# Kernel optimization log

Measured on AMD Instinct MI355X. Metric: run time of the kernel, lower is better.

## Reference

```python
import jax, jax.numpy as jnp
import numpy as np

COMMIT_LAMBDA = 0.25


def setup_inputs() -> dict:
    key = jax.random.key(0)
    k1, k2 = jax.random.split(key)
    B, C, T = 8, 256, 1024
    NCB, K, D = 2, 8192, 128
    x = jax.random.normal(k1, (B, C, T), dtype=jnp.float32)
    # EMA codebook weights buffer (init: randn * 0.1)
    codebooks = jax.random.normal(k2, (NCB, K, D), dtype=jnp.float32) * 0.1
    return {"x": x, "codebooks": codebooks}


def reference(x, codebooks):
    B, C, T = x.shape
    ncb, K, d = codebooks.shape
    # [B, C, T] -> [B*T, ncb, d]
    xs = x.reshape(B, ncb, d, T).transpose(0, 3, 1, 2).reshape(B * T, ncb, d)
    # squared euclidean distances (argmin-equivalent to cdist)
    x2 = jnp.sum(xs * xs, axis=-1)[..., None]            # [N, ncb, 1]
    c2 = jnp.sum(codebooks * codebooks, axis=-1)[None]    # [1, ncb, K]
    xc = jnp.einsum('bnd,nkd->bnk', xs, codebooks)        # [N, ncb, K]
    d2 = x2 - 2.0 * xc + c2
    idx = jnp.argmin(d2, axis=-1)                         # [N, ncb] int
    # gather nearest code vectors: [N, ncb, d]
    q = codebooks[jnp.arange(ncb)[None, :], idx]
    # straight-through estimator
    q_st = xs + jax.lax.stop_gradient(q - xs)
    # commitment loss (training mode): sum over codebooks of mse(x_i, q_i.detach())
    loss = COMMIT_LAMBDA * jnp.sum(
        jnp.mean((xs - jax.lax.stop_gradient(q)) ** 2, axis=(0, 2))
    )
    # reassemble to [B, C, T]
    quantized = q_st.reshape(B, T, ncb, d).transpose(0, 2, 3, 1).reshape(B, C, T)
    indices = idx.reshape(B, T, ncb).transpose(0, 2, 1)   # [B, ncb, T]
    return quantized, indices, loss
```

## Files before the change

### kernel.cpp

```cpp
#include <hip/hip_runtime.h>
#include <hip/hip_bf16.h>

#define BB   8
#define TT   1024
#define NCBN 2
#define DD   128
#define KK   8192
#define MM   8192

constexpr int OUT_IDX_OFF  = BB * 256 * TT;
constexpr int OUT_LOSS_OFF = OUT_IDX_OFF + BB * NCBN * TT;

#define THR   0.45f
#define QCAP  2048

typedef __attribute__((ext_vector_type(8))) short   short8;
typedef __attribute__((ext_vector_type(4))) float   float4v;

__device__ __forceinline__ unsigned short f2bf(float v) {
    unsigned u = __float_as_uint(v);
    return (unsigned short)((u + 0x7FFFu + ((u >> 16) & 1u)) >> 16);
}

__device__ __forceinline__ unsigned short f2bf_dn(float v) {
    unsigned u = __float_as_uint(v);
    unsigned short h = (unsigned short)(u >> 16);
    if ((u & 0x80000000u) && (u & 0xFFFFu)) ++h;
    return h;
}

__device__ __forceinline__ void gl_lds16(const void* g, void* l) {
    __builtin_amdgcn_global_load_lds(
        (const __attribute__((address_space(1))) unsigned int*)g,
        (__attribute__((address_space(3))) unsigned int*)l, 16, 0, 0);
}

__global__ __launch_bounds__(256)
void pack_x_kernel(const float* __restrict__ x, unsigned short* __restrict__ xbf,
                   float* __restrict__ x2, unsigned long long* __restrict__ pmin) {
    __shared__ float Ld[DD][65];
    const int b = blockIdx.x >> 1, n = blockIdx.x & 1;
    const int t0 = blockIdx.y * 64;
    const int tid = threadIdx.x;

    const float* base = x + ((size_t)(b * 256 + n * 128)) * TT + t0;
    const int dro = tid >> 2, q4 = tid & 3;
#pragma unroll
    for (int half = 0; half < 2; ++half) {
        int d = dro + half * 64;
        const float* rp = base + (size_t)d * TT + q4 * 16;
#pragma unroll
        for (int j = 0; j < 4; ++j) {
            float4 v = *(const float4*)(rp + j * 4);
            int t = q4 * 16 + j * 4;
            Ld[d][t + 0] = v.x; Ld[d][t + 1] = v.y;
            Ld[d][t + 2] = v.z; Ld[d][t + 3] = v.w;
        }
    }
    __syncthreads();

    if (tid < 64) {
        float s = 0.f;
        for (int d = 0; d < DD; ++d) { float v = Ld[d][tid]; s = fmaf(v, v, s); }
        x2[(size_t)n * MM + b * TT + t0 + tid] = s;
        pmin[(size_t)n * MM + b * TT + t0 + tid] = 0xFFFFFFFFFFFFFFFFull;
    }

    unsigned short* orow0 = xbf + ((size_t)n * MM + b * TT + t0) * DD;
#pragma unroll
    for (int pp = 0; pp < 4; ++pp) {
        int u = tid + pp * 256;
        int tt = u >> 4, sg = u & 15;
        unsigned short tmp[8];
#pragma unroll
        for (int j = 0; j < 8; ++j) tmp[j] = f2bf(Ld[sg * 8 + j][tt]);
        uint4 pk;
        pk.x = (unsigned)tmp[0] | ((unsigned)tmp[1] << 16);
        pk.y = (unsigned)tmp[2] | ((unsigned)tmp[3] << 16);
        pk.z = (unsigned)tmp[4] | ((unsigned)tmp[5] << 16);
        pk.w = (unsigned)tmp[6] | ((unsigned)tmp[7] << 16);
        *(uint4*)(orow0 + (size_t)tt * DD + sg * 8) = pk;
    }
}

__global__ __launch_bounds__(256)
void pack_c_kernel(const float* __restrict__ cb, unsigned short* __restrict__ cbf,
                   float* __restrict__ c2, float* __restrict__ out) {
    int g = blockIdx.x * 256 + threadIdx.x;
    if (g == 0) out[OUT_LOSS_OFF] = 0.f;
    const float4* crow = (const float4*)(cb + (size_t)g * DD);
    unsigned short* orow = cbf + (size_t)g * DD;
    float s = 0.f;
#pragma unroll 4
    for (int i2 = 0; i2 < 16; ++i2) {
        float4 v0 = crow[2 * i2];
        float4 v1 = crow[2 * i2 + 1];
        s = fmaf(v0.x, v0.x, s); s = fmaf(v0.y, v0.y, s);
        s = fmaf(v0.z, v0.z, s); s = fmaf(v0.w, v0.w, s);
        s = fmaf(v1.x, v1.x, s); s = fmaf(v1.y, v1.y, s);
        s = fmaf(v1.z, v1.z, s); s = fmaf(v1.w, v1.w, s);
        uint4 pk;
        pk.x = (unsigned)f2bf(v0.x) | ((unsigned)f2bf(v0.y) << 16);
        pk.y = (unsigned)f2bf(v0.z) | ((unsigned)f2bf(v0.w) << 16);
        pk.z = (unsigned)f2bf(v1.x) | ((unsigned)f2bf(v1.y) << 16);
        pk.w = (unsigned)f2bf(v1.z) | ((unsigned)f2bf(v1.w) << 16);
        *(uint4*)(orow + i2 * 8) = pk;
    }
    c2[g] = s;
}

__device__ void rescore_one(int n, int m, int k,
                            const float* __restrict__ x, const float* __restrict__ cb,
                            const float* __restrict__ x2, const float* __restrict__ c2,
                            unsigned long long* __restrict__ pmin) {
    int b = m >> 10, t = m & (TT - 1);
    const float* xp = x + ((size_t)(b * 256 + n * 128)) * TT + t;
    const float* cp = cb + ((size_t)(n * KK + k)) * DD;
    float xc = 0.f;
    for (int d = 0; d < DD; ++d)
        xc = fmaf(xp[(size_t)d * TT], cp[d], xc);
    float u = x2[n * MM + m] - 2.0f * xc;
    float s = u + c2[n * KK + k];
    unsigned long long pk = ((unsigned long long)__float_as_uint(s) << 32) | (unsigned)k;
    atomicMin(pmin + (size_t)n * MM + m, pk);
}

__global__ __launch_bounds__(512, 4)
void screen_kernel(const unsigned short* __restrict__ xbf,
                   const unsigned short* __restrict__ cbf,
                   const float* __restrict__ c2,
                   const float* __restrict__ x,
                   const float* __restrict__ cb32,
                   const float* __restrict__ x2,
                   unsigned long long* __restrict__ pmin) {
    __shared__ __align__(16) unsigned short Csh[2][128 * 128];
    __shared__ float          c2s[2][128];
    __shared__ unsigned int   minU[128];
    __shared__ unsigned int   qcnt;
    __shared__ unsigned int   queue[QCAP];
    __shared__ unsigned short queueY[QCAP];

    const int tid = threadIdx.x;
    const int id  = blockIdx.x;
    const int n   = id & 1;
    const int ks  = (id >> 1) & 3;
    const int qt  = id >> 3;
    const int m0  = qt * 128;
    const int k0  = ks * 2048;

    const int wave = tid >> 6, lane = tid & 63;
    const int cw = wave & 1, qw = wave >> 1;
    const int quad = lane >> 4, l15 = lane & 15;

    int goff[4];
#pragma unroll
    for (int p = 0; p < 4; ++p) {
        int u   = (p * 8 + wave) * 64 + lane;
        int row = u >> 4;
        int seg = (u & 15) ^ (row & 15);
        goff[p] = (row * DD + seg * 8) * 2;
    }

    const char*  asrc0 = (const char*)(cbf + ((size_t)n * KK + k0) * DD);
    const float* c2p   = c2 + (size_t)n * KK + k0;

    {
        const char* qsrc = (const char*)(xbf + ((size_t)n * MM + m0) * DD);
#pragma unroll
        for (int p = 0; p < 4; ++p)
            gl_lds16(qsrc + goff[p], &Csh[0][(p * 8 + wave) * 512]);
#pragma unroll
        for (int p = 0; p < 4; ++p)
            gl_lds16(asrc0 + goff[p], &Csh[1][(p * 8 + wave) * 512]);
    }
    if (tid < 32)  *(float4*)&c2s[1][tid * 4] = *(const float4*)(c2p + tid * 4);
    if (tid < 128) minU[tid] = 0xFFFFFFFFu;
    if (tid == 0)  qcnt = 0;
    __syncthreads();

    short8 bfr[2][4];
#pragma unroll
    for (int tq = 0; tq < 2; ++tq) {
        int q = qw * 32 + tq * 16 + l15;
#pragma unroll
        for (int k4 = 0; k4 < 4; ++k4) {
            int seg = k4 * 4 + quad;
            bfr[tq][k4] = *(const short8*)(&Csh[0][q * 128 + ((seg ^ l15) * 8)]);
        }
    }
    __syncthreads();

    float thr[2] = {3.4e38f, 3.4e38f};

    for (int it = 0; it <= 16; ++it) {
        const int sb   = it & 1;
        const int cbuf = sb ^ 1;
        const int dcur = (it < 16) ? it : 0;

        if (it < 16) {
            const int dn = (it + 1 < 16) ? (it + 1) : 0;
            const char* src = asrc0 + (size_t)dn * (128 * DD * 2);
#pragma unroll
            for (int p = 0; p < 4; ++p)
                gl_lds16(src + goff[p], &Csh[sb][(p * 8 + wave) * 512]);
            if (tid < 32)
                *(float4*)&c2s[sb][tid * 4] =
                    *(const float4*)(c2p + dn * 128 + tid * 4);
        }

        float4v acc[4][2];
#pragma unroll
        for (int tc = 0; tc < 4; ++tc)
#pragma unroll
            for (int tq = 0; tq < 2; ++tq)
                acc[tc][tq] = (float4v){0.f, 0.f, 0.f, 0.f};

#pragma unroll
        for (int k4 = 0; k4 < 4; ++k4) {
            short8 a[4];
#pragma unroll
            for (int tc = 0; tc < 4; ++tc) {
                int r = cw * 64 + tc * 16 + l15;
                int seg = k4 * 4 + quad;
                a[tc] = *(const short8*)(&Csh[cbuf][r * 128 + ((seg ^ l15) * 8)]);
            }
#pragma unroll
            for (int tc = 0; tc < 4; ++tc)
#pragma unroll
                for (int tq = 0; tq < 2; ++tq)
                    acc[tc][tq] = __builtin_amdgcn_mfma_f32_16x16x32_bf16(
                        a[tc], bfr[tq][k4], acc[tc][tq], 0, 0, 0);
        }

        float cmin[2] = {3.4e38f, 3.4e38f};
        const bool enq = (it > 0);
#pragma unroll
        for (int tc = 0; tc < 4; ++tc) {
            float4v c2r = *(const float4v*)(&c2s[cbuf][cw * 64 + tc * 16 + quad * 4]);
#pragma unroll
            for (int tq = 0; tq < 2; ++tq) {
                float y0 = fmaf(-2.0f, acc[tc][tq][0], c2r[0]);
                float y1 = fmaf(-2.0f, acc[tc][tq][1], c2r[1]);
                float y2 = fmaf(-2.0f, acc[tc][tq][2], c2r[2]);
                float y3 = fmaf(-2.0f, acc[tc][tq][3], c2r[3]);
                float m4 = fminf(fminf(y0, y1), fminf(y2, y3));
                cmin[tq] = fminf(cmin[tq], m4);
                if (enq && m4 <= thr[tq]) {
                    float yv[4] = {y0, y1, y2, y3};
#pragma unroll
                    for (int rg = 0; rg < 4; ++rg) {
                        if (yv[rg] <= thr[tq]) {
                            unsigned idx  = atomicAdd(&qcnt, 1u);
                            unsigned code = (unsigned)(dcur * 128 + cw * 64 + tc * 16 + quad * 4 + rg);
                            unsigned q    = (unsigned)(qw * 32 + tq * 16 + l15);
                            if (idx < QCAP) {
                                queue[idx]  = (q << 11) | code;
                                queueY[idx] = f2bf_dn(yv[rg]);
                            } else {
                                rescore_one(n, m0 + (int)q, k0 + (int)code,
                                            x, cb32, x2, c2, pmin);
                            }
                        }
                    }
                }
            }
        }

        if (it < 16) {
#pragma unroll
            for (int tq = 0; tq < 2; ++tq) {
                float v = cmin[tq];
                v = fminf(v, __shfl_xor(v, 16, 64));
                v = fminf(v, __shfl_xor(v, 32, 64));
                if (quad == 0) {
                    unsigned u  = __float_as_uint(v);
                    unsigned mu = (u & 0x80000000u) ? ~u : (u | 0x80000000u);
                    atomicMin(&minU[qw * 32 + tq * 16 + l15], mu);
                }
            }
        }
        __syncthreads();
        if (it < 16) {
#pragma unroll
            for (int tq = 0; tq < 2; ++tq) {
                unsigned mu = minU[qw * 32 + tq * 16 + l15];
                unsigned u  = (mu & 0x80000000u) ? (mu & 0x7FFFFFFFu) : ~mu;
                thr[tq] = __uint_as_float(u) + THR;
            }
        }
    }

    unsigned total = qcnt; if (total > QCAP) total = QCAP;
    for (unsigned i = tid; i < total; i += 512) {
        unsigned ent = queue[i];
        unsigned q   = ent >> 11;
        unsigned mu  = minU[q];
        unsigned u   = (mu & 0x80000000u) ? (mu & 0x7FFFFFFFu) : ~mu;
        float thrF   = __uint_as_float(u) + THR;
        float yv     = __uint_as_float((unsigned)queueY[i] << 16);
        if (yv <= thrF)
            rescore_one(n, m0 + (int)q, k0 + (int)(ent & 2047u),
                        x, cb32, x2, c2, pmin);
    }
}

__global__ __launch_bounds__(256)
void gather_kernel(const float* __restrict__ x, const float* __restrict__ cb,
                   const unsigned long long* __restrict__ pmin,
                   float* __restrict__ out) {
    __shared__ float Cr[64][DD + 1];
    __shared__ int   kid[64];
    const int b = blockIdx.x >> 1, n = blockIdx.x & 1;
    const int t0 = blockIdx.y * 64;
    const int tid = threadIdx.x;

    if (tid < 64) {
        int t = t0 + tid;
        int k = (int)(pmin[(size_t)n * MM + b * TT + t] & 0xFFFFFFFFull);
        kid[tid] = k;
        out[OUT_IDX_OFF + (b * NCBN + n) * TT + t] = (float)k;
    }
    __syncthreads();

    {
        int row = tid >> 2, q4 = tid & 3;
        const float* cp = cb + ((size_t)n * KK + kid[row]) * DD + q4 * 32;
#pragma unroll
        for (int j = 0; j < 8; ++j) {
            float4 v = *(const float4*)(cp + j * 4);
            int d = q4 * 32 + j * 4;
            Cr[row][d + 0] = v.x; Cr[row][d + 1] = v.y;
            Cr[row][d + 2] = v.z; Cr[row][d + 3] = v.w;
        }
    }
    __syncthreads();

    float lsum = 0.f;
    const float* xb = x  + ((size_t)(b * 256 + n * 128)) * TT + t0;
    float*       ob = out + ((size_t)(b * 256 + n * 128)) * TT + t0;
#pragma unroll
    for (int pp = 0; pp < 8; ++pp) {
        int u  = tid + pp * 256;
        int d  = u >> 4, ts = (u & 15) * 4;
        float4 xv = *(const float4*)(xb + (size_t)d * TT + ts);
        float4 qv = { Cr[ts + 0][d], Cr[ts + 1][d], Cr[ts + 2][d], Cr[ts + 3][d] };
        *(float4*)(ob + (size_t)d * TT + ts) = qv;
        float e;
        e = xv.x - qv.x; lsum = fmaf(e, e, lsum);
        e = xv.y - qv.y; lsum = fmaf(e, e, lsum);
        e = xv.z - qv.z; lsum = fmaf(e, e, lsum);
        e = xv.w - qv.w; lsum = fmaf(e, e, lsum);
    }

#pragma unroll
    for (int o = 32; o > 0; o >>= 1) lsum += __shfl_down(lsum, o, 64);
    __shared__ float wsum[4];
    int lane = tid & 63, w = tid >> 6;
    if (lane == 0) wsum[w] = lsum;
    __syncthreads();
    if (tid == 0) {
        float tot = wsum[0] + wsum[1] + wsum[2] + wsum[3];
        atomicAdd(out + OUT_LOSS_OFF, tot * 2.384185791015625e-7f);
    }
}

extern "C" void kernel_launch(void* const* d_in, const int* in_sizes, int n_in,
                              void* d_out, int out_size, void* d_ws, size_t ws_size,
                              hipStream_t stream) {
    (void)in_sizes; (void)n_in; (void)out_size; (void)ws_size;
    const float* x  = (const float*)d_in[0];
    const float* cb = (const float*)d_in[1];
    float* out = (float*)d_out;

    char* ws = (char*)d_ws;
    unsigned short* xbf = (unsigned short*)(ws);
    unsigned short* cbf = (unsigned short*)(ws + (4u << 20));
    float* x2 = (float*)(ws + (8u << 20));
    float* c2 = (float*)(ws + (8u << 20) + (64u << 10));
    unsigned long long* pmin =
        (unsigned long long*)(ws + (8u << 20) + (128u << 10));

    pack_x_kernel<<<dim3(16, 16), 256, 0, stream>>>(x, xbf, x2, pmin);
    pack_c_kernel<<<dim3(64), 256, 0, stream>>>(cb, cbf, c2, out);

    screen_kernel<<<dim3(512), 512, 0, stream>>>(xbf, cbf, c2, x, cb, x2, pmin);
    gather_kernel<<<dim3(16, 16), 256, 0, stream>>>(x, cb, pmin, out);
}
```

Baseline: 191.0 us.

## Fuse pack kernels, tighten per-tile threshold, drop pipeline tail, spill queue overflow

Merges the x and codebook packing kernels into one launch. In the screen kernel, each tile's scores are computed first and reduced to a per-tile minimum, so candidates are filtered against min(running threshold, tile min + margin) from the first tile onward instead of skipping enqueue on the first pass. The extra 17th loop iteration is removed. Queue overflow now goes to a per-block global spill buffer instead of immediate fp32 rescoring. The aim is fewer candidates to rescore and one less launch, at the cost of holding scores in registers and adding spill-buffer global traffic.

```diff
diff --git a/kernel.cpp b/kernel.cpp
--- a/kernel.cpp
+++ b/kernel.cpp
@@ -13,6 +13,7 @@
 
 #define THR   0.45f
 #define QCAP  2048
+#define SCAP  2048
 
 typedef __attribute__((ext_vector_type(8))) short   short8;
 typedef __attribute__((ext_vector_type(4))) float   float4v;
@@ -36,77 +37,80 @@
 }
 
 __global__ __launch_bounds__(256)
-void pack_x_kernel(const float* __restrict__ x, unsigned short* __restrict__ xbf,
-                   float* __restrict__ x2, unsigned long long* __restrict__ pmin) {
+void pack_kernel(const float* __restrict__ x, const float* __restrict__ cb,
+                 unsigned short* __restrict__ xbf, unsigned short* __restrict__ cbf,
+                 float* __restrict__ x2, float* __restrict__ c2,
+                 unsigned long long* __restrict__ pmin, float* __restrict__ out) {
     __shared__ float Ld[DD][65];
-    const int b = blockIdx.x >> 1, n = blockIdx.x & 1;
-    const int t0 = blockIdx.y * 64;
+    const int gb  = blockIdx.x;
     const int tid = threadIdx.x;
 
-    const float* base = x + ((size_t)(b * 256 + n * 128)) * TT + t0;
-    const int dro = tid >> 2, q4 = tid & 3;
-#pragma unroll
-    for (int half = 0; half < 2; ++half) {
-        int d = dro + half * 64;
-        const float* rp = base + (size_t)d * TT + q4 * 16;
-#pragma unroll
-        for (int j = 0; j < 4; ++j) {
-            float4 v = *(const float4*)(rp + j * 4);
-            int t = q4 * 16 + j * 4;
-            Ld[d][t + 0] = v.x; Ld[d][t + 1] = v.y;
-            Ld[d][t + 2] = v.z; Ld[d][t + 3] = v.w;
-        }
-    }
-    __syncthreads();
-
-    if (tid < 64) {
+    if (gb < 256) {
+        const int bxn = gb & 15, ty = gb >> 4;
+        const int b = bxn >> 1, n = bxn & 1;
+        const int t0 = ty * 64;
+
+        const float* base = x + ((size_t)(b * 256 + n * 128)) * TT + t0;
+        const int dro = tid >> 2, q4 = tid & 3;
+#pragma unroll
+        for (int half = 0; half < 2; ++half) {
+            int d = dro + half * 64;
+            const float* rp = base + (size_t)d * TT + q4 * 16;
+#pragma unroll
+            for (int j = 0; j < 4; ++j) {
+                float4 v = *(const float4*)(rp + j * 4);
+                int t = q4 * 16 + j * 4;
+                Ld[d][t + 0] = v.x; Ld[d][t + 1] = v.y;
+                Ld[d][t + 2] = v.z; Ld[d][t + 3] = v.w;
+            }
+        }
+        __syncthreads();
+
+        if (tid < 64) {
+            float s = 0.f;
+            for (int d = 0; d < DD; ++d) { float v = Ld[d][tid]; s = fmaf(v, v, s); }
+            x2[(size_t)n * MM + b * TT + t0 + tid] = s;
+            pmin[(size_t)n * MM + b * TT + t0 + tid] = 0xFFFFFFFFFFFFFFFFull;
+        }
+
+        unsigned short* orow0 = xbf + ((size_t)n * MM + b * TT + t0) * DD;
+#pragma unroll
+        for (int pp = 0; pp < 4; ++pp) {
+            int u = tid + pp * 256;
+            int tt = u >> 4, sg = u & 15;
+            unsigned short tmp[8];
+#pragma unroll
+            for (int j = 0; j < 8; ++j) tmp[j] = f2bf(Ld[sg * 8 + j][tt]);
+            uint4 pk;
+            pk.x = (unsigned)tmp[0] | ((unsigned)tmp[1] << 16);
+            pk.y = (unsigned)tmp[2] | ((unsigned)tmp[3] << 16);
+            pk.z = (unsigned)tmp[4] | ((unsigned)tmp[5] << 16);
+            pk.w = (unsigned)tmp[6] | ((unsigned)tmp[7] << 16);
+            *(uint4*)(orow0 + (size_t)tt * DD + sg * 8) = pk;
+        }
+    } else {
+        int g = (gb - 256) * 256 + tid;
+        if (g == 0) out[OUT_LOSS_OFF] = 0.f;
+        const float4* crow = (const float4*)(cb + (size_t)g * DD);
+        unsigned short* orow = cbf + (size_t)g * DD;
         float s = 0.f;
-        for (int d = 0; d < DD; ++d) { float v = Ld[d][tid]; s = fmaf(v, v, s); }
-        x2[(size_t)n * MM + b * TT + t0 + tid] = s;
-        pmin[(size_t)n * MM + b * TT + t0 + tid] = 0xFFFFFFFFFFFFFFFFull;
-    }
-
-    unsigned short* orow0 = xbf + ((size_t)n * MM + b * TT + t0) * DD;
-#pragma unroll
-    for (int pp = 0; pp < 4; ++pp) {
-        int u = tid + pp * 256;
-        int tt = u >> 4, sg = u & 15;
-        unsigned short tmp[8];
-#pragma unroll
-        for (int j = 0; j < 8; ++j) tmp[j] = f2bf(Ld[sg * 8 + j][tt]);
-        uint4 pk;
-        pk.x = (unsigned)tmp[0] | ((unsigned)tmp[1] << 16);
-        pk.y = (unsigned)tmp[2] | ((unsigned)tmp[3] << 16);
-        pk.z = (unsigned)tmp[4] | ((unsigned)tmp[5] << 16);
-        pk.w = (unsigned)tmp[6] | ((unsigned)tmp[7] << 16);
-        *(uint4*)(orow0 + (size_t)tt * DD + sg * 8) = pk;
-    }
-}
-
-__global__ __launch_bounds__(256)
-void pack_c_kernel(const float* __restrict__ cb, unsigned short* __restrict__ cbf,
-                   float* __restrict__ c2, float* __restrict__ out) {
-    int g = blockIdx.x * 256 + threadIdx.x;
-    if (g == 0) out[OUT_LOSS_OFF] = 0.f;
-    const float4* crow = (const float4*)(cb + (size_t)g * DD);
-    unsigned short* orow = cbf + (size_t)g * DD;
-    float s = 0.f;
 #pragma unroll 4
-    for (int i2 = 0; i2 < 16; ++i2) {
-        float4 v0 = crow[2 * i2];
-        float4 v1 = crow[2 * i2 + 1];
-        s = fmaf(v0.x, v0.x, s); s = fmaf(v0.y, v0.y, s);
-        s = fmaf(v0.z, v0.z, s); s = fmaf(v0.w, v0.w, s);
-        s = fmaf(v1.x, v1.x, s); s = fmaf(v1.y, v1.y, s);
-        s = fmaf(v1.z, v1.z, s); s = fmaf(v1.w, v1.w, s);
-        uint4 pk;
-        pk.x = (unsigned)f2bf(v0.x) | ((unsigned)f2bf(v0.y) << 16);
-        pk.y = (unsigned)f2bf(v0.z) | ((unsigned)f2bf(v0.w) << 16);
-        pk.z = (unsigned)f2bf(v1.x) | ((unsigned)f2bf(v1.y) << 16);
-        pk.w = (unsigned)f2bf(v1.z) | ((unsigned)f2bf(v1.w) << 16);
-        *(uint4*)(orow + i2 * 8) = pk;
-    }
-    c2[g] = s;
+        for (int i2 = 0; i2 < 16; ++i2) {
+            float4 v0 = crow[2 * i2];
+            float4 v1 = crow[2 * i2 + 1];
+            s = fmaf(v0.x, v0.x, s); s = fmaf(v0.y, v0.y, s);
+            s = fmaf(v0.z, v0.z, s); s = fmaf(v0.w, v0.w, s);
+            s = fmaf(v1.x, v1.x, s); s = fmaf(v1.y, v1.y, s);
+            s = fmaf(v1.z, v1.z, s); s = fmaf(v1.w, v1.w, s);
+            uint4 pk;
+            pk.x = (unsigned)f2bf(v0.x) | ((unsigned)f2bf(v0.y) << 16);
+            pk.y = (unsigned)f2bf(v0.z) | ((unsigned)f2bf(v0.w) << 16);
+            pk.z = (unsigned)f2bf(v1.x) | ((unsigned)f2bf(v1.y) << 16);
+            pk.w = (unsigned)f2bf(v1.z) | ((unsigned)f2bf(v1.w) << 16);
+            *(uint4*)(orow + i2 * 8) = pk;
+        }
+        c2[g] = s;
+    }
 }
 
 __device__ void rescore_one(int n, int m, int k,
@@ -132,7 +136,8 @@
                    const float* __restrict__ x,
                    const float* __restrict__ cb32,
                    const float* __restrict__ x2,
-                   unsigned long long* __restrict__ pmin) {
+                   unsigned long long* __restrict__ pmin,
+                   unsigned long long* __restrict__ spill, int scap) {
     __shared__ __align__(16) unsigned short Csh[2][128 * 128];
     __shared__ float          c2s[2][128];
     __shared__ unsigned int   minU[128];
@@ -152,6 +157,8 @@
     const int cw = wave & 1, qw = wave >> 1;
     const int quad = lane >> 4, l15 = lane & 15;
 
+    unsigned long long* spillp = spill + (size_t)id * (size_t)(scap > 0 ? scap : 1);
+
     int goff[4];
 #pragma unroll
     for (int p = 0; p < 4; ++p) {
@@ -192,13 +199,12 @@
 
     float thr[2] = {3.4e38f, 3.4e38f};
 
-    for (int it = 0; it <= 16; ++it) {
+    for (int it = 0; it < 16; ++it) {
         const int sb   = it & 1;
         const int cbuf = sb ^ 1;
-        const int dcur = (it < 16) ? it : 0;
-
-        if (it < 16) {
-            const int dn = (it + 1 < 16) ? (it + 1) : 0;
+
+        if (it < 15) {
+            const int dn = it + 1;
             const char* src = asrc0 + (size_t)dn * (128 * DD * 2);
 #pragma unroll
             for (int p = 0; p < 4; ++p)
@@ -233,7 +239,6 @@
         }
 
         float cmin[2] = {3.4e38f, 3.4e38f};
-        const bool enq = (it > 0);
 #pragma unroll
         for (int tc = 0; tc < 4; ++tc) {
             float4v c2r = *(const float4v*)(&c2s[cbuf][cw * 64 + tc * 16 + quad * 4]);
@@ -243,19 +248,44 @@
                 float y1 = fmaf(-2.0f, acc[tc][tq][1], c2r[1]);
                 float y2 = fmaf(-2.0f, acc[tc][tq][2], c2r[2]);
                 float y3 = fmaf(-2.0f, acc[tc][tq][3], c2r[3]);
-                float m4 = fminf(fminf(y0, y1), fminf(y2, y3));
-                cmin[tq] = fminf(cmin[tq], m4);
-                if (enq && m4 <= thr[tq]) {
-                    float yv[4] = {y0, y1, y2, y3};
+                acc[tc][tq] = (float4v){y0, y1, y2, y3};
+                cmin[tq] = fminf(cmin[tq],
+                                 fminf(fminf(y0, y1), fminf(y2, y3)));
+            }
+        }
+#pragma unroll
+        for (int tq = 0; tq < 2; ++tq) {
+            float v = cmin[tq];
+            v = fminf(v, __shfl_xor(v, 16, 64));
+            v = fminf(v, __shfl_xor(v, 32, 64));
+            cmin[tq] = v;
+        }
+
+        float te[2];
+#pragma unroll
+        for (int tq = 0; tq < 2; ++tq)
+            te[tq] = fminf(thr[tq], cmin[tq] + THR);
+#pragma unroll
+        for (int tc = 0; tc < 4; ++tc) {
+#pragma unroll
+            for (int tq = 0; tq < 2; ++tq) {
+                float4v yv = acc[tc][tq];
+                float m4 = fminf(fminf(yv[0], yv[1]), fminf(yv[2], yv[3]));
+                if (m4 <= te[tq]) {
 #pragma unroll
                     for (int rg = 0; rg < 4; ++rg) {
-                        if (yv[rg] <= thr[tq]) {
+                        if (yv[rg] <= te[tq]) {
                             unsigned idx  = atomicAdd(&qcnt, 1u);
-                            unsigned code = (unsigned)(dcur * 128 + cw * 64 + tc * 16 + quad * 4 + rg);
+                            unsigned code = (unsigned)(it * 128 + cw * 64 + tc * 16 + quad * 4 + rg);
                             unsigned q    = (unsigned)(qw * 32 + tq * 16 + l15);
+                            unsigned ent  = (q << 11) | code;
                             if (idx < QCAP) {
-                                queue[idx]  = (q << 11) | code;
+                                queue[idx]  = ent;
                                 queueY[idx] = f2bf_dn(yv[rg]);
+                            } else if ((int)(idx - QCAP) < scap) {
+                                spillp[idx - QCAP] =
+                                    ((unsigned long long)ent << 32) |
+                                    (unsigned long long)f2bf_dn(yv[rg]);
                             } else {
                                 rescore_one(n, m0 + (int)q, k0 + (int)code,
                                             x, cb32, x2, c2, pmin);
@@ -266,21 +296,16 @@
             }
         }
 
-        if (it < 16) {
-#pragma unroll
-            for (int tq = 0; tq < 2; ++tq) {
-                float v = cmin[tq];
-                v = fminf(v, __shfl_xor(v, 16, 64));
-                v = fminf(v, __shfl_xor(v, 32, 64));
-                if (quad == 0) {
-                    unsigned u  = __float_as_uint(v);
-                    unsigned mu = (u & 0x80000000u) ? ~u : (u | 0x80000000u);
-                    atomicMin(&minU[qw * 32 + tq * 16 + l15], mu);
-                }
+#pragma unroll
+        for (int tq = 0; tq < 2; ++tq) {
+            if (quad == 0) {
+                unsigned u  = __float_as_uint(cmin[tq]);
+                unsigned mu = (u & 0x80000000u) ? ~u : (u | 0x80000000u);
+                atomicMin(&minU[qw * 32 + tq * 16 + l15], mu);
             }
         }
         __syncthreads();
-        if (it < 16) {
+        if (it < 15) {
 #pragma unroll
             for (int tq = 0; tq < 2; ++tq) {
                 unsigned mu = minU[qw * 32 + tq * 16 + l15];
@@ -290,14 +315,21 @@
         }
     }
 
-    unsigned total = qcnt; if (total > QCAP) total = QCAP;
+    unsigned total = qcnt;
+    unsigned cap = (unsigned)(QCAP + (scap > 0 ? scap : 0));
+    if (total > cap) total = cap;
     for (unsigned i = tid; i < total; i += 512) {
-        unsigned ent = queue[i];
+        unsigned ent; unsigned short y16;
+        if (i < QCAP) { ent = queue[i]; y16 = queueY[i]; }
+        else {
+            unsigned long long se = spillp[i - QCAP];
+            ent = (unsigned)(se >> 32); y16 = (unsigned short)se;
+        }
         unsigned q   = ent >> 11;
         unsigned mu  = minU[q];
         unsigned u   = (mu & 0x80000000u) ? (mu & 0x7FFFFFFFu) : ~mu;
         float thrF   = __uint_as_float(u) + THR;
-        float yv     = __uint_as_float((unsigned)queueY[i] << 16);
+        float yv     = __uint_as_float((unsigned)y16 << 16);
         if (yv <= thrF)
             rescore_one(n, m0 + (int)q, k0 + (int)(ent & 2047u),
                         x, cb32, x2, c2, pmin);
@@ -367,7 +399,7 @@
 extern "C" void kernel_launch(void* const* d_in, const int* in_sizes, int n_in,
                               void* d_out, int out_size, void* d_ws, size_t ws_size,
                               hipStream_t stream) {
-    (void)in_sizes; (void)n_in; (void)out_size; (void)ws_size;
+    (void)in_sizes; (void)n_in; (void)out_size;
     const float* x  = (const float*)d_in[0];
     const float* cb = (const float*)d_in[1];
     float* out = (float*)d_out;
@@ -379,10 +411,17 @@
     float* c2 = (float*)(ws + (8u << 20) + (64u << 10));
     unsigned long long* pmin =
         (unsigned long long*)(ws + (8u << 20) + (128u << 10));
-
-    pack_x_kernel<<<dim3(16, 16), 256, 0, stream>>>(x, xbf, x2, pmin);
-    pack_c_kernel<<<dim3(64), 256, 0, stream>>>(cb, cbf, c2, out);
-
-    screen_kernel<<<dim3(512), 512, 0, stream>>>(xbf, cbf, c2, x, cb, x2, pmin);
+    size_t spill_off = (8u << 20) + (256u << 10);
+    unsigned long long* spill = (unsigned long long*)(ws + spill_off);
+
+    int scap = 0;
+    if (ws_size > spill_off) {
+        size_t per_block = (ws_size - spill_off) / (512ull * 8ull);
+        scap = (int)(per_block > SCAP ? SCAP : per_block);
+    }
+
+    pack_kernel<<<dim3(320), 256, 0, stream>>>(x, cb, xbf, cbf, x2, c2, pmin, out);
+    screen_kernel<<<dim3(512), 512, 0, stream>>>(xbf, cbf, c2, x, cb, x2, pmin,
+                                                 spill, scap);
     gather_kernel<<<dim3(16, 16), 256, 0, stream>>>(x, cb, pmin, out);
 }
```

Result: slower. 256.0 us (+34.0%).
